# Kernel optimization log

Measured on AMD Instinct MI355X. Metric: run time of the kernel, lower is better.

## Reference

```python
import jax, jax.numpy as jnp
import numpy as np

N_NODES = 50000
N_EDGES = 800000
IN_DIM = 128
HID = 64
HEADS = 4
OUT_DIM = 128
NEG_SLOPE = 0.2


def setup_inputs() -> dict:
    key = jax.random.key(0)
    ks = jax.random.split(key, 11)
    x = jax.random.normal(ks[0], (N_NODES, IN_DIM), dtype=jnp.float32)
    edge_index = jax.random.randint(ks[1], (2, N_EDGES), 0, N_NODES, dtype=jnp.int64)
    s1 = 1.0 / np.sqrt(IN_DIM)
    s2 = 1.0 / np.sqrt(HEADS * HID)
    W1 = jax.random.normal(ks[2], (IN_DIM, HEADS * HID), dtype=jnp.float32) * s1
    a_src1 = jax.random.normal(ks[3], (HEADS, HID), dtype=jnp.float32) * s2
    a_dst1 = jax.random.normal(ks[4], (HEADS, HID), dtype=jnp.float32) * s2
    b1 = jnp.zeros((HEADS * HID,), dtype=jnp.float32)
    W2 = jax.random.normal(ks[5], (HEADS * HID, OUT_DIM), dtype=jnp.float32) * s2
    a_src2 = jax.random.normal(ks[6], (1, OUT_DIM), dtype=jnp.float32) * 0.1
    a_dst2 = jax.random.normal(ks[7], (1, OUT_DIM), dtype=jnp.float32) * 0.1
    b2 = jnp.zeros((OUT_DIM,), dtype=jnp.float32)
    return {"x": x, "edge_index": edge_index, "W1": W1, "a_src1": a_src1,
            "a_dst1": a_dst1, "b1": b1, "W2": W2, "a_src2": a_src2,
            "a_dst2": a_dst2, "b2": b2}


def _gat_conv(x, src, dst, W, a_src, a_dst, bias, heads, out_per_head, concat):
    n = x.shape[0]
    # linear projection per head: [N, H, F]
    h = (x @ W).reshape(n, heads, out_per_head)
    # per-node attention terms: [N, H]
    alpha_src = jnp.einsum('nhf,hf->nh', h, a_src)
    alpha_dst = jnp.einsum('nhf,hf->nh', h, a_dst)
    # edge logits with LeakyReLU: [E, H]
    e = jax.nn.leaky_relu(alpha_src[src] + alpha_dst[dst], NEG_SLOPE)
    # softmax over incoming edges of each destination node
    m = jax.ops.segment_max(e, dst, num_segments=n)  # [N, H]
    m = jnp.where(jnp.isfinite(m), m, 0.0)
    e = jnp.exp(e - m[dst])
    denom = jax.ops.segment_sum(e, dst, num_segments=n)  # [N, H]
    alpha = e / (denom[dst] + 1e-16)  # [E, H]
    # weighted scatter-aggregate of source messages
    out = jax.ops.segment_sum(h[src] * alpha[:, :, None], dst, num_segments=n)  # [N, H, F]
    if concat:
        out = out.reshape(n, heads * out_per_head)
    else:
        out = out.mean(axis=1)
    return out + bias


def reference(x, edge_index, W1, a_src1, a_dst1, b1, W2, a_src2, a_dst2, b2):
    n = x.shape[0]
    # PyG GATConv adds self-loops by default
    loops = jnp.arange(n, dtype=edge_index.dtype)
    src = jnp.concatenate([edge_index[0], loops])
    dst = jnp.concatenate([edge_index[1], loops])
    # dropout layers are identity in inference
    h = _gat_conv(x, src, dst, W1, a_src1, a_dst1, b1, HEADS, HID, True)
    h = jax.nn.elu(h)
    out = _gat_conv(h, src, dst, W2, a_src2, a_dst2, b2, 1, OUT_DIM, True)
    # F.normalize(p=2, dim=1)
    norm = jnp.linalg.norm(out, axis=1, keepdims=True)
    return out / jnp.maximum(norm, 1e-12)
```

## Files before the change

### kernel.cpp

```cpp
#include <hip/hip_runtime.h>
#include <hip/hip_fp16.h>
#include <math.h>

#define N_NODES 50000
#define N_EDGES 800000
#define ET (N_EDGES + N_NODES)
#define IN_DIM 128
#define HID 64
#define HEADS 4
#define C1 (HEADS * HID)
#define OUT_DIM 128
#define NEG_SLOPE 0.2f
#define MTILES 3125
#define SCAN_B 1024
#define NSCB 49

typedef _Float16 h8 __attribute__((ext_vector_type(8)));
typedef float f4 __attribute__((ext_vector_type(4)));

__device__ __forceinline__ float leaky(float v) { return fmaxf(v, NEG_SLOPE * v); }
__device__ __forceinline__ float elu(float v) { return v > 0.0f ? v : expm1f(v); }

__device__ __forceinline__ void fma_mix8(float* acc, h8 v, float w) {
    union { h8 h; int i[4]; } u; u.h = v;
#pragma unroll
    for (int k = 0; k < 4; ++k) {
        asm("v_fma_mix_f32 %0, %1, %2, %0 op_sel:[0,0,0] op_sel_hi:[1,0,0]"
            : "+v"(acc[2 * k]) : "v"(u.i[k]), "v"(w));
        asm("v_fma_mix_f32 %0, %1, %2, %0 op_sel:[1,0,0] op_sel_hi:[1,0,0]"
            : "+v"(acc[2 * k + 1]) : "v"(u.i[k]), "v"(w));
    }
}

__global__ void prep_kernel(const float* __restrict__ W1, const float* __restrict__ W2,
                            const int* __restrict__ dst, __half* __restrict__ w1t,
                            __half* __restrict__ w2t, int* __restrict__ cnt) {
    const int tid = blockIdx.x * blockDim.x + threadIdx.x;
    const int np = gridDim.x * blockDim.x;
    for (int i = tid; i < IN_DIM * C1; i += np) {
        int k1 = i >> 8, n1 = i & 255;
        w1t[n1 * IN_DIM + k1] = __float2half(W1[i]);
        int k2 = i >> 7, n2 = i & 127;
        w2t[n2 * C1 + k2] = __float2half(W2[i]);
    }
    for (int i = tid; i < ET; i += np) {
        int d = (i < N_EDGES) ? dst[i] : i - N_EDGES;
        atomicAdd(&cnt[d], 1);
    }
}

__global__ void scan_local(const int* __restrict__ cnt, int* __restrict__ lscan,
                           int* __restrict__ bsum) {
    __shared__ int wsum[16];
    const int t = threadIdx.x, lane = t & 63, wv = t >> 6;
    int idx = blockIdx.x * SCAN_B + t;
    int v = (idx < N_NODES) ? cnt[idx] : 0;
    int sc = v;
#pragma unroll
    for (int o = 1; o < 64; o <<= 1) {
        int u = __shfl_up(sc, o);
        if (lane >= o) sc += u;
    }
    if (lane == 63) wsum[wv] = sc;
    __syncthreads();
    if (t == 0) {
        int run = 0;
#pragma unroll
        for (int w = 0; w < 16; ++w) { int s = wsum[w]; wsum[w] = run; run += s; }
        bsum[blockIdx.x] = run;
    }
    __syncthreads();
    if (idx < N_NODES) lscan[idx] = sc + wsum[wv];
}

__global__ void scan_bsum(int* __restrict__ bsum) {
    const int t = threadIdx.x;
    int v = (t < NSCB) ? bsum[t] : 0;
    int sc = v;
#pragma unroll
    for (int o = 1; o < 64; o <<= 1) {
        int u = __shfl_up(sc, o);
        if (t >= o) sc += u;
    }
    if (t < NSCB) bsum[t] = sc - v;
}

__global__ void scan_final(const int* __restrict__ cnt, const int* __restrict__ lscan,
                           const int* __restrict__ bsum, int* __restrict__ rp,
                           int* __restrict__ cursor) {
    int idx = blockIdx.x * SCAN_B + threadIdx.x;
    if (idx == 0) rp[0] = 0;
    if (idx >= N_NODES) return;
    int inc = lscan[idx] + bsum[idx >> 10];
    rp[idx + 1] = inc;
    cursor[idx] = inc - cnt[idx];
}

__global__ void scatter_kernel(const int* __restrict__ src, const int* __restrict__ dst,
                               int* __restrict__ cursor, int* __restrict__ col_src) {
    int i = blockIdx.x * blockDim.x + threadIdx.x;
    if (i >= ET) return;
    int s, d;
    if (i < N_EDGES) { s = src[i]; d = dst[i]; } else { s = d = i - N_EDGES; }
    int pos = atomicAdd(&cursor[d], 1);
    col_src[pos] = s;
}

__global__ __launch_bounds__(256) void gemm1_mfma(
        const float* __restrict__ x, const __half* __restrict__ w1t,
        const float* __restrict__ aws, const float* __restrict__ awd,
        __half* __restrict__ h, float* __restrict__ as1, float* __restrict__ ad1) {
    const int tile = blockIdx.x * 4 + (threadIdx.x >> 6);
    if (tile >= MTILES) return;
    const int lane = threadIdx.x & 63;
    const int m0 = tile * 16, lm = lane & 15, lq = lane >> 4;
    h8 afrag[4];
    const float4* xrow = (const float4*)(x + (size_t)(m0 + lm) * IN_DIM + lq * 8);
#pragma unroll
    for (int kt = 0; kt < 4; ++kt) {
        float4 a = xrow[kt * 8];
        float4 b = xrow[kt * 8 + 1];
        union { h8 v; __half2 p[4]; } u;
        u.p[0] = __floats2half2_rn(a.x, a.y);
        u.p[1] = __floats2half2_rn(a.z, a.w);
        u.p[2] = __floats2half2_rn(b.x, b.y);
        u.p[3] = __floats2half2_rn(b.z, b.w);
        afrag[kt] = u.v;
    }
    f4 acc[16];
#pragma unroll
    for (int nt = 0; nt < 16; ++nt) acc[nt] = (f4){0.f, 0.f, 0.f, 0.f};
#pragma unroll
    for (int nt = 0; nt < 16; ++nt) {
        const h8* brow = (const h8*)(w1t + (size_t)(nt * 16 + lm) * IN_DIM + lq * 8);
#pragma unroll
        for (int kt = 0; kt < 4; ++kt)
            acc[nt] = __builtin_amdgcn_mfma_f32_16x16x32_f16(afrag[kt], brow[kt * 4],
                                                             acc[nt], 0, 0, 0);
    }
    float sS[4][4] = {{0.f}}, sD[4][4] = {{0.f}};
#pragma unroll
    for (int nt = 0; nt < 16; ++nt) {
        int col = nt * 16 + lm;
        float wa = aws[col], wd = awd[col];
        int hd = nt >> 2;
#pragma unroll
        for (int r = 0; r < 4; ++r) {
            float v = acc[nt][r];
            h[(size_t)(m0 + lq * 4 + r) * C1 + col] = __float2half(v);
            sS[hd][r] += v * wa;
            sD[hd][r] += v * wd;
        }
    }
#pragma unroll
    for (int o = 1; o < 16; o <<= 1) {
#pragma unroll
        for (int hd = 0; hd < 4; ++hd)
#pragma unroll
            for (int r = 0; r < 4; ++r) {
                sS[hd][r] += __shfl_xor(sS[hd][r], o);
                sD[hd][r] += __shfl_xor(sD[hd][r], o);
            }
    }
    if (lm == 0) {
#pragma unroll
        for (int r = 0; r < 4; ++r) {
            int row = m0 + lq * 4 + r;
            ((float4*)as1)[row] = make_float4(sS[0][r], sS[1][r], sS[2][r], sS[3][r]);
            ((float4*)ad1)[row] = make_float4(sD[0][r], sD[1][r], sD[2][r], sD[3][r]);
        }
    }
}

__global__ __launch_bounds__(256) void gemm2_mfma(
        const __half* __restrict__ ah, const __half* __restrict__ w2t,
        const float* __restrict__ aws, const float* __restrict__ awd,
        __half* __restrict__ h, float* __restrict__ as2, float* __restrict__ ad2) {
    const int tile = blockIdx.x * 4 + (threadIdx.x >> 6);
    if (tile >= MTILES) return;
    const int lane = threadIdx.x & 63;
    const int m0 = tile * 16, lm = lane & 15, lq = lane >> 4;
    h8 afrag[8];
    const h8* arow = (const h8*)(ah + (size_t)(m0 + lm) * C1 + lq * 8);
#pragma unroll
    for (int kt = 0; kt < 8; ++kt) afrag[kt] = arow[kt * 4];
    f4 acc[8];
#pragma unroll
    for (int nt = 0; nt < 8; ++nt) acc[nt] = (f4){0.f, 0.f, 0.f, 0.f};
#pragma unroll
    for (int nt = 0; nt < 8; ++nt) {
        const h8* brow = (const h8*)(w2t + (size_t)(nt * 16 + lm) * C1 + lq * 8);
#pragma unroll
        for (int kt = 0; kt < 8; ++kt)
            acc[nt] = __builtin_amdgcn_mfma_f32_16x16x32_f16(afrag[kt], brow[kt * 4],
                                                             acc[nt], 0, 0, 0);
    }
    float sS[4] = {0.f, 0.f, 0.f, 0.f}, sD[4] = {0.f, 0.f, 0.f, 0.f};
#pragma unroll
    for (int nt = 0; nt < 8; ++nt) {
        int col = nt * 16 + lm;
        float wa = aws[col], wd = awd[col];
#pragma unroll
        for (int r = 0; r < 4; ++r) {
            float v = acc[nt][r];
            h[(size_t)(m0 + lq * 4 + r) * OUT_DIM + col] = __float2half(v);
            sS[r] += v * wa;
            sD[r] += v * wd;
        }
    }
#pragma unroll
    for (int o = 1; o < 16; o <<= 1) {
#pragma unroll
        for (int r = 0; r < 4; ++r) {
            sS[r] += __shfl_xor(sS[r], o);
            sD[r] += __shfl_xor(sD[r], o);
        }
    }
    if (lm == 0) {
#pragma unroll
        for (int r = 0; r < 4; ++r) {
            int row = m0 + lq * 4 + r;
            as2[row] = sS[r];
            ad2[row] = sD[r];
        }
    }
}

__global__ __launch_bounds__(256) void aggregate1_fused(
        const int* __restrict__ rp, const int* __restrict__ cs,
        const __half* __restrict__ h1h, const float* __restrict__ as1,
        const float* __restrict__ ad1, const float* __restrict__ b1,
        __half* __restrict__ out1h) {
    __shared__ int2 stg[8][32][4];
    const int hw = threadIdx.x >> 5, li = threadIdx.x & 31;
    const int d = blockIdx.x * 8 + hw;
    const int e0 = rp[d], deg = rp[d + 1] - e0;
    const float4 adv = ((const float4*)ad1)[d];
    const int head = li >> 3;
    const int lbyte = li * 16;
    const char* hbase = (const char*)h1h;
    int2* sp = &stg[hw][0][0];
    float acc[8] = {0.f, 0.f, 0.f, 0.f, 0.f, 0.f, 0.f, 0.f};
    float4 dsum = make_float4(0.f, 0.f, 0.f, 0.f);
    for (int c0 = 0; c0 < deg; c0 += 32) {
        const int clen = min(32, deg - c0);
        int idx = c0 + li;
        bool valid = idx < deg;
        int s = valid ? cs[e0 + idx] : 0;
        float4 av = ((const float4*)as1)[s];
        float x0 = valid ? __expf(leaky(av.x + adv.x)) : 0.f;
        float x1 = valid ? __expf(leaky(av.y + adv.y)) : 0.f;
        float x2 = valid ? __expf(leaky(av.z + adv.z)) : 0.f;
        float x3 = valid ? __expf(leaky(av.w + adv.w)) : 0.f;
        int off = valid ? (s << 9) : 0;
        ((int4*)sp)[li * 2]     = make_int4(off, __float_as_int(x0), off, __float_as_int(x1));
        ((int4*)sp)[li * 2 + 1] = make_int4(off, __float_as_int(x2), off, __float_as_int(x3));
        dsum.x += x0; dsum.y += x1; dsum.z += x2; dsum.w += x3;
        __builtin_amdgcn_wave_barrier();
        int j = 0;
        for (; j + 2 <= clen; j += 2) {
            int2 p0 = sp[j * 4 + head];
            int2 p1 = sp[(j + 1) * 4 + head];
            h8 v0 = *(const h8*)(hbase + p0.x + lbyte);
            h8 v1 = *(const h8*)(hbase + p1.x + lbyte);
            fma_mix8(acc, v0, __int_as_float(p0.y));
            fma_mix8(acc, v1, __int_as_float(p1.y));
        }
        if (j < clen) {
            int2 p0 = sp[j * 4 + head];
            h8 v0 = *(const h8*)(hbase + p0.x + lbyte);
            fma_mix8(acc, v0, __int_as_float(p0.y));
        }
        __builtin_amdgcn_wave_barrier();
    }
#pragma unroll
    for (int o = 16; o > 0; o >>= 1) {
        dsum.x += __shfl_xor(dsum.x, o); dsum.y += __shfl_xor(dsum.y, o);
        dsum.z += __shfl_xor(dsum.z, o); dsum.w += __shfl_xor(dsum.w, o);
    }
    float den = (head == 0) ? dsum.x : (head == 1) ? dsum.y : (head == 2) ? dsum.z : dsum.w;
    float inv = 1.0f / (den + 1e-16f);
    float4 bA = ((const float4*)b1)[li * 2];
    float4 bB = ((const float4*)b1)[li * 2 + 1];
    h8 o;
    o[0] = (_Float16)elu(acc[0] * inv + bA.x);
    o[1] = (_Float16)elu(acc[1] * inv + bA.y);
    o[2] = (_Float16)elu(acc[2] * inv + bA.z);
    o[3] = (_Float16)elu(acc[3] * inv + bA.w);
    o[4] = (_Float16)elu(acc[4] * inv + bB.x);
    o[5] = (_Float16)elu(acc[5] * inv + bB.y);
    o[6] = (_Float16)elu(acc[6] * inv + bB.z);
    o[7] = (_Float16)elu(acc[7] * inv + bB.w);
    *(h8*)((char*)out1h + (size_t)d * 512 + lbyte) = o;
}

__global__ __launch_bounds__(256) void aggregate2_fused(
        const int* __restrict__ rp, const int* __restrict__ cs,
        const __half* __restrict__ h2h, const float* __restrict__ as2,
        const float* __restrict__ ad2, const float* __restrict__ b2,
        float* __restrict__ out) {
    __shared__ int2 stg[8][32];
    const int hw = threadIdx.x >> 5, li = threadIdx.x & 31;
    const int d = blockIdx.x * 8 + hw;
    const int e0 = rp[d], deg = rp[d + 1] - e0;
    const float adv = ad2[d];
    const int q = li >> 4, lo = li & 15;
    const int lbyte = lo * 16;
    const char* hbase = (const char*)h2h;
    float acc[8] = {0.f, 0.f, 0.f, 0.f, 0.f, 0.f, 0.f, 0.f};
    float dsum = 0.f;
    for (int c0 = 0; c0 < deg; c0 += 32) {
        const int clen = min(32, deg - c0);
        int idx = c0 + li;
        bool valid = idx < deg;
        int s = valid ? cs[e0 + idx] : 0;
        float x = valid ? __expf(leaky(as2[s] + adv)) : 0.f;
        stg[hw][li] = make_int2(valid ? (s << 8) : 0, __float_as_int(x));
        dsum += x;
        __builtin_amdgcn_wave_barrier();
        int j = 0;
        for (; j + 4 <= clen; j += 4) {
            int2 p0 = stg[hw][j + q];
            int2 p1 = stg[hw][j + 2 + q];
            h8 v0 = *(const h8*)(hbase + p0.x + lbyte);
            h8 v1 = *(const h8*)(hbase + p1.x + lbyte);
            fma_mix8(acc, v0, __int_as_float(p0.y));
            fma_mix8(acc, v1, __int_as_float(p1.y));
        }
        for (; j < clen; j += 2) {
            int2 p0 = stg[hw][j + q];
            h8 v0 = *(const h8*)(hbase + p0.x + lbyte);
            fma_mix8(acc, v0, __int_as_float(p0.y));
        }
        __builtin_amdgcn_wave_barrier();
    }
#pragma unroll
    for (int f = 0; f < 8; ++f) acc[f] += __shfl_xor(acc[f], 16);
#pragma unroll
    for (int o = 16; o > 0; o >>= 1) dsum += __shfl_xor(dsum, o);
    if (q == 0) {
        float inv = 1.0f / (dsum + 1e-16f);
        float4 bA = ((const float4*)b2)[lo * 2];
        float4 bB = ((const float4*)b2)[lo * 2 + 1];
        float v0 = acc[0] * inv + bA.x, v1 = acc[1] * inv + bA.y;
        float v2 = acc[2] * inv + bA.z, v3 = acc[3] * inv + bA.w;
        float v4 = acc[4] * inv + bB.x, v5 = acc[5] * inv + bB.y;
        float v6 = acc[6] * inv + bB.z, v7 = acc[7] * inv + bB.w;
        float ss = v0 * v0 + v1 * v1 + v2 * v2 + v3 * v3 +
                   v4 * v4 + v5 * v5 + v6 * v6 + v7 * v7;
#pragma unroll
        for (int o = 1; o < 16; o <<= 1) ss += __shfl_xor(ss, o);
        float sc = 1.0f / fmaxf(sqrtf(ss), 1e-12f);
        float4* orow = (float4*)((char*)out + (size_t)d * 512 + lo * 32);
        orow[0] = make_float4(v0 * sc, v1 * sc, v2 * sc, v3 * sc);
        orow[1] = make_float4(v4 * sc, v5 * sc, v6 * sc, v7 * sc);
    }
}

extern "C" void kernel_launch(void* const* d_in, const int* in_sizes, int n_in,
                              void* d_out, int out_size, void* d_ws, size_t ws_size,
                              hipStream_t stream) {
    const float* x     = (const float*)d_in[0];
    const int*   edge  = (const int*)d_in[1];
    const int*   src   = edge;
    const int*   dst   = edge + N_EDGES;
    const float* W1    = (const float*)d_in[2];
    const float* aw_s1 = (const float*)d_in[3];
    const float* aw_d1 = (const float*)d_in[4];
    const float* b1    = (const float*)d_in[5];
    const float* W2    = (const float*)d_in[6];
    const float* aw_s2 = (const float*)d_in[7];
    const float* aw_d2 = (const float*)d_in[8];
    const float* b2    = (const float*)d_in[9];
    float* out = (float*)d_out;

    char* ws = (char*)d_ws;
    size_t off = 0;
    auto alloc = [&](size_t bytes) {
        void* p = ws + off;
        off += (bytes + 255) & ~(size_t)255;
        return p;
    };
    int*    col_src = (int*)alloc((size_t)ET * 4);
    int*    rp     = (int*)alloc((size_t)(N_NODES + 1) * 4);
    int*    cursor = (int*)alloc((size_t)N_NODES * 4);
    int*    cnt    = (int*)alloc((size_t)N_NODES * 4);
    int*    lscan  = (int*)alloc((size_t)NSCB * SCAN_B * 4);
    int*    bsum   = (int*)alloc((size_t)NSCB * 4);
    float*  as1    = (float*)alloc((size_t)N_NODES * HEADS * 4);
    float*  ad1    = (float*)alloc((size_t)N_NODES * HEADS * 4);
    float*  as2    = (float*)alloc((size_t)N_NODES * 4);
    float*  ad2    = (float*)alloc((size_t)N_NODES * 4);
    __half* w1t    = (__half*)alloc((size_t)IN_DIM * C1 * 2);
    __half* w2t    = (__half*)alloc((size_t)C1 * OUT_DIM * 2);
    __half* h1h    = (__half*)alloc((size_t)N_NODES * C1 * 2);
    __half* out1h  = (__half*)alloc((size_t)N_NODES * C1 * 2);
    __half* h2h    = h1h;
    (void)off;

    hipMemsetAsync(cnt, 0, (size_t)N_NODES * 4, stream);

    const int egrid = (ET + 255) / 256;

    prep_kernel<<<1024, 256, 0, stream>>>(W1, W2, dst, w1t, w2t, cnt);
    scan_local<<<NSCB, SCAN_B, 0, stream>>>(cnt, lscan, bsum);
    scan_bsum<<<1, 64, 0, stream>>>(bsum);
    scan_final<<<NSCB, SCAN_B, 0, stream>>>(cnt, lscan, bsum, rp, cursor);
    scatter_kernel<<<egrid, 256, 0, stream>>>(src, dst, cursor, col_src);

    gemm1_mfma<<<(MTILES + 3) / 4, 256, 0, stream>>>(x, w1t, aw_s1, aw_d1, h1h, as1, ad1);
    aggregate1_fused<<<N_NODES / 8, 256, 0, stream>>>(rp, col_src, h1h, as1, ad1, b1, out1h);

    gemm2_mfma<<<(MTILES + 3) / 4, 256, 0, stream>>>(out1h, w2t, aw_s2, aw_d2, h2h, as2, ad2);
    aggregate2_fused<<<N_NODES / 8, 256, 0, stream>>>(rp, col_src, h2h, as2, ad2, b2, out);
}
```

Baseline: 350.1 us.

## Split layer-1 features into head-major planes and aggregate one head per block

GEMM1 now stores the projected features and the per-node attention terms in head-major planes (one N×64 plane per head) rather than node-major rows. Aggregation for layer 1 launches four times as many blocks, each handling a single head, and processes four edges at a time per half-wave with 16-byte feature loads. Partial sums are then reduced across lanes with shuffles. The aim is to make each head's gathered working set smaller and more cache-friendly and to raise parallelism, at the cost of redundant CSR index reads per head and extra cross-lane reductions.

Result: no change. 356.4 us (+1.8%).

```diff
diff --git a/kernel.cpp b/kernel.cpp
--- a/kernel.cpp
+++ b/kernel.cpp
@@ -109,7 +109,7 @@
 __global__ __launch_bounds__(256) void gemm1_mfma(
         const float* __restrict__ x, const __half* __restrict__ w1t,
         const float* __restrict__ aws, const float* __restrict__ awd,
-        __half* __restrict__ h, float* __restrict__ as1, float* __restrict__ ad1) {
+        __half* __restrict__ hm, float* __restrict__ as1m, float* __restrict__ ad1m) {
     const int tile = blockIdx.x * 4 + (threadIdx.x >> 6);
     if (tile >= MTILES) return;
     const int lane = threadIdx.x & 63;
@@ -144,10 +144,11 @@
         int col = nt * 16 + lm;
         float wa = aws[col], wd = awd[col];
         int hd = nt >> 2;
+        int f = col & 63;
 #pragma unroll
         for (int r = 0; r < 4; ++r) {
             float v = acc[nt][r];
-            h[(size_t)(m0 + lq * 4 + r) * C1 + col] = __float2half(v);
+            hm[((size_t)hd * N_NODES + (m0 + lq * 4 + r)) * 64 + f] = __float2half(v);
             sS[hd][r] += v * wa;
             sD[hd][r] += v * wd;
         }
@@ -166,8 +167,11 @@
 #pragma unroll
         for (int r = 0; r < 4; ++r) {
             int row = m0 + lq * 4 + r;
-            ((float4*)as1)[row] = make_float4(sS[0][r], sS[1][r], sS[2][r], sS[3][r]);
-            ((float4*)ad1)[row] = make_float4(sD[0][r], sD[1][r], sD[2][r], sD[3][r]);
+#pragma unroll
+            for (int hd = 0; hd < 4; ++hd) {
+                as1m[hd * N_NODES + row] = sS[hd][r];
+                ad1m[hd * N_NODES + row] = sD[hd][r];
+            }
         }
     }
 }
@@ -228,70 +232,68 @@
 
 __global__ __launch_bounds__(256) void aggregate1_fused(
         const int* __restrict__ rp, const int* __restrict__ cs,
-        const __half* __restrict__ h1h, const float* __restrict__ as1,
-        const float* __restrict__ ad1, const float* __restrict__ b1,
+        const __half* __restrict__ h1hm, const float* __restrict__ as1m,
+        const float* __restrict__ ad1m, const float* __restrict__ b1,
         __half* __restrict__ out1h) {
-    __shared__ int2 stg[8][32][4];
+    __shared__ int2 stg[8][32];
+    const int head = blockIdx.x & 3, g = blockIdx.x >> 2;
     const int hw = threadIdx.x >> 5, li = threadIdx.x & 31;
-    const int d = blockIdx.x * 8 + hw;
+    const int d = g * 8 + hw;
     const int e0 = rp[d], deg = rp[d + 1] - e0;
-    const float4 adv = ((const float4*)ad1)[d];
-    const int head = li >> 3;
-    const int lbyte = li * 16;
-    const char* hbase = (const char*)h1h;
-    int2* sp = &stg[hw][0][0];
+    const float* asb = as1m + head * N_NODES;
+    const float adv = ad1m[head * N_NODES + d];
+    const char* hb = (const char*)h1hm + (size_t)head * N_NODES * 128;
+    const int es = li >> 3, fl = li & 7;
+    const int lbyte = fl * 16;
     float acc[8] = {0.f, 0.f, 0.f, 0.f, 0.f, 0.f, 0.f, 0.f};
-    float4 dsum = make_float4(0.f, 0.f, 0.f, 0.f);
+    float dsum = 0.f;
     for (int c0 = 0; c0 < deg; c0 += 32) {
         const int clen = min(32, deg - c0);
         int idx = c0 + li;
         bool valid = idx < deg;
         int s = valid ? cs[e0 + idx] : 0;
-        float4 av = ((const float4*)as1)[s];
-        float x0 = valid ? __expf(leaky(av.x + adv.x)) : 0.f;
-        float x1 = valid ? __expf(leaky(av.y + adv.y)) : 0.f;
-        float x2 = valid ? __expf(leaky(av.z + adv.z)) : 0.f;
-        float x3 = valid ? __expf(leaky(av.w + adv.w)) : 0.f;
-        int off = valid ? (s << 9) : 0;
-        ((int4*)sp)[li * 2]     = make_int4(off, __float_as_int(x0), off, __float_as_int(x1));
-        ((int4*)sp)[li * 2 + 1] = make_int4(off, __float_as_int(x2), off, __float_as_int(x3));
-        dsum.x += x0; dsum.y += x1; dsum.z += x2; dsum.w += x3;
+        float x = valid ? __expf(leaky(asb[s] + adv)) : 0.f;
+        stg[hw][li] = make_int2(s << 7, __float_as_int(x));
+        dsum += x;
         __builtin_amdgcn_wave_barrier();
         int j = 0;
-        for (; j + 2 <= clen; j += 2) {
-            int2 p0 = sp[j * 4 + head];
-            int2 p1 = sp[(j + 1) * 4 + head];
-            h8 v0 = *(const h8*)(hbase + p0.x + lbyte);
-            h8 v1 = *(const h8*)(hbase + p1.x + lbyte);
+        for (; j + 8 <= clen; j += 8) {
+            int2 p0 = stg[hw][j + es];
+            int2 p1 = stg[hw][j + 4 + es];
+            h8 v0 = *(const h8*)(hb + p0.x + lbyte);
+            h8 v1 = *(const h8*)(hb + p1.x + lbyte);
             fma_mix8(acc, v0, __int_as_float(p0.y));
             fma_mix8(acc, v1, __int_as_float(p1.y));
         }
-        if (j < clen) {
-            int2 p0 = sp[j * 4 + head];
-            h8 v0 = *(const h8*)(hbase + p0.x + lbyte);
+        for (; j < clen; j += 4) {
+            int2 p0 = stg[hw][j + es];
+            h8 v0 = *(const h8*)(hb + p0.x + lbyte);
             fma_mix8(acc, v0, __int_as_float(p0.y));
         }
         __builtin_amdgcn_wave_barrier();
     }
 #pragma unroll
-    for (int o = 16; o > 0; o >>= 1) {
-        dsum.x += __shfl_xor(dsum.x, o); dsum.y += __shfl_xor(dsum.y, o);
-        dsum.z += __shfl_xor(dsum.z, o); dsum.w += __shfl_xor(dsum.w, o);
-    }
-    float den = (head == 0) ? dsum.x : (head == 1) ? dsum.y : (head == 2) ? dsum.z : dsum.w;
-    float inv = 1.0f / (den + 1e-16f);
-    float4 bA = ((const float4*)b1)[li * 2];
-    float4 bB = ((const float4*)b1)[li * 2 + 1];
-    h8 o;
-    o[0] = (_Float16)elu(acc[0] * inv + bA.x);
-    o[1] = (_Float16)elu(acc[1] * inv + bA.y);
-    o[2] = (_Float16)elu(acc[2] * inv + bA.z);
-    o[3] = (_Float16)elu(acc[3] * inv + bA.w);
-    o[4] = (_Float16)elu(acc[4] * inv + bB.x);
-    o[5] = (_Float16)elu(acc[5] * inv + bB.y);
-    o[6] = (_Float16)elu(acc[6] * inv + bB.z);
-    o[7] = (_Float16)elu(acc[7] * inv + bB.w);
-    *(h8*)((char*)out1h + (size_t)d * 512 + lbyte) = o;
+    for (int f = 0; f < 8; ++f) {
+        acc[f] += __shfl_xor(acc[f], 8);
+        acc[f] += __shfl_xor(acc[f], 16);
+    }
+#pragma unroll
+    for (int o = 16; o > 0; o >>= 1) dsum += __shfl_xor(dsum, o);
+    if (es == 0) {
+        float inv = 1.0f / (dsum + 1e-16f);
+        float4 bA = ((const float4*)b1)[head * 16 + fl * 2];
+        float4 bB = ((const float4*)b1)[head * 16 + fl * 2 + 1];
+        h8 o;
+        o[0] = (_Float16)elu(acc[0] * inv + bA.x);
+        o[1] = (_Float16)elu(acc[1] * inv + bA.y);
+        o[2] = (_Float16)elu(acc[2] * inv + bA.z);
+        o[3] = (_Float16)elu(acc[3] * inv + bA.w);
+        o[4] = (_Float16)elu(acc[4] * inv + bB.x);
+        o[5] = (_Float16)elu(acc[5] * inv + bB.y);
+        o[6] = (_Float16)elu(acc[6] * inv + bB.z);
+        o[7] = (_Float16)elu(acc[7] * inv + bB.w);
+        *(h8*)((char*)out1h + (size_t)d * 512 + head * 128 + lbyte) = o;
+    }
 }
 
 __global__ __launch_bounds__(256) void aggregate2_fused(
@@ -393,9 +395,9 @@
     float*  ad2    = (float*)alloc((size_t)N_NODES * 4);
     __half* w1t    = (__half*)alloc((size_t)IN_DIM * C1 * 2);
     __half* w2t    = (__half*)alloc((size_t)C1 * OUT_DIM * 2);
-    __half* h1h    = (__half*)alloc((size_t)N_NODES * C1 * 2);
+    __half* h1hm   = (__half*)alloc((size_t)N_NODES * C1 * 2);
     __half* out1h  = (__half*)alloc((size_t)N_NODES * C1 * 2);
-    __half* h2h    = h1h;
+    __half* h2h    = h1hm;
     (void)off;
 
     hipMemsetAsync(cnt, 0, (size_t)N_NODES * 4, stream);
@@ -408,8 +410,8 @@
     scan_final<<<NSCB, SCAN_B, 0, stream>>>(cnt, lscan, bsum, rp, cursor);
     scatter_kernel<<<egrid, 256, 0, stream>>>(src, dst, cursor, col_src);
 
-    gemm1_mfma<<<(MTILES + 3) / 4, 256, 0, stream>>>(x, w1t, aw_s1, aw_d1, h1h, as1, ad1);
-    aggregate1_fused<<<N_NODES / 8, 256, 0, stream>>>(rp, col_src, h1h, as1, ad1, b1, out1h);
+    gemm1_mfma<<<(MTILES + 3) / 4, 256, 0, stream>>>(x, w1t, aw_s1, aw_d1, h1hm, as1, ad1);
+    aggregate1_fused<<<(N_NODES / 8) * HEADS, 256, 0, stream>>>(rp, col_src, h1hm, as1, ad1, b1, out1h);
 
     gemm2_mfma<<<(MTILES + 3) / 4, 256, 0, stream>>>(out1h, w2t, aw_s2, aw_d2, h2h, as2, ad2);
     aggregate2_fused<<<N_NODES / 8, 256, 0, stream>>>(rp, col_src, h2h, as2, ad2, b2, out);
```
